# Performance work log

Hardware: AMD Instinct MI355X
Metric: run time of the kernel (lower is better)

Reference implementation:

```python
import jax, jax.numpy as jnp
import numpy as np
import math

NUM_HEADS = 8
RES_K = 9  # res_kernel_size


def setup_inputs() -> dict:
    key = jax.random.key(0)
    ks = jax.random.split(key, 6)
    N, C, h, w = 8, 256, 64, 64
    x = jax.random.normal(ks[0], (N, C, h, w), dtype=jnp.float32)
    w_qkv = jax.random.normal(ks[1], (3 * C, C), dtype=jnp.float32) * 0.02
    b_qkv = jax.random.normal(ks[2], (3 * C,), dtype=jnp.float32) * 0.02
    w_proj = jax.random.normal(ks[3], (C, C), dtype=jnp.float32) * 0.02
    b_proj = jax.random.normal(ks[4], (C,), dtype=jnp.float32) * 0.02
    w_dconv = jax.random.normal(ks[5], (NUM_HEADS, 1, RES_K, 1), dtype=jnp.float32) * 0.1
    return {"x": x, "w_qkv": w_qkv, "b_qkv": b_qkv,
            "w_proj": w_proj, "b_proj": b_proj, "w_dconv": w_dconv}


def _l2norm(t):
    # torch x / x.norm(dim=-1, keepdim=True): plain L2 norm, no eps
    return t / jnp.linalg.norm(t, axis=-1, keepdims=True)


def reference(x, w_qkv, b_qkv, w_proj, b_proj, w_dconv):
    N, C, h, w = x.shape
    H = NUM_HEADS
    D = C // H
    L = h * w
    xt = x.reshape(N, C, L).transpose(0, 2, 1)  # [N, L, C]
    qkv = xt @ w_qkv.T + b_qkv                   # [N, L, 3C]
    qkv = qkv.reshape(N, L, 3, H, D).transpose(2, 0, 3, 1, 4)  # [3, N, H, L, D]
    q, k, v = qkv[0], qkv[1], qkv[2]
    q = _l2norm(q)
    k = _l2norm(k)
    # depthwise conv over token dim: v as NCHW with C=H, H=L, W=D
    pad = RES_K // 2
    dconv_v = jax.lax.conv_general_dilated(
        v, w_dconv, window_strides=(1, 1), padding=[(pad, pad), (0, 0)],
        dimension_numbers=("NCHW", "OIHW", "NCHW"), feature_group_count=H)
    attn = jnp.einsum("nhld,nhle->nhde", k, v)   # [N, H, D, D]
    out = 0.5 * v + (1.0 / math.pi) * jnp.einsum("nhld,nhde->nhle", q, attn)
    out = _l2norm(out)
    out = out + dconv_v
    out = out.transpose(0, 2, 1, 3).reshape(N, L, C)  # [N, L, C]
    out = out @ w_proj.T + b_proj
    return out.transpose(0, 2, 1).reshape(N, C, h, w)
```

## Files before the change

### kernel.cpp

```cpp
#include <hip/hip_runtime.h>

#define NB 8
#define CC 256
#define HH 8
#define DD 32
#define LL 4096

typedef short v8s __attribute__((ext_vector_type(8)));
typedef float v4f __attribute__((ext_vector_type(4)));
typedef unsigned short v8u __attribute__((ext_vector_type(8)));
typedef unsigned short v4us __attribute__((ext_vector_type(4)));

__device__ __forceinline__ float4 ld4(const float* p) { return *(const float4*)p; }

__device__ __forceinline__ unsigned short f2bf(float f) {
    union { float f; unsigned int u; } v; v.f = f;
    unsigned int r = (v.u + 0x7FFFu + ((v.u >> 16) & 1u)) >> 16;
    return (unsigned short)r;
}
__device__ __forceinline__ float bf2f(unsigned short u) {
    union { unsigned int u; float f; } v; v.u = ((unsigned int)u) << 16;
    return v.f;
}

__device__ __forceinline__ void gl_lds16(const unsigned short* g, unsigned short* l) {
    __builtin_amdgcn_global_load_lds(
        (const __attribute__((address_space(1))) void*)g,
        (__attribute__((address_space(3))) void*)l, 16, 0, 0);
}

__global__ __launch_bounds__(256) void prep_w(
    const float* __restrict__ wq, const float* __restrict__ wp,
    unsigned short* __restrict__ dwq, unsigned short* __restrict__ dwp)
{
    int ti = blockIdx.x * 256 + threadIdx.x;
    if (ti < 24576) {
        int i = ti * 8;
        float4 f0 = ld4(wq + i), f1 = ld4(wq + i + 4);
        v8u o;
        o[0] = f2bf(f0.x); o[1] = f2bf(f0.y); o[2] = f2bf(f0.z); o[3] = f2bf(f0.w);
        o[4] = f2bf(f1.x); o[5] = f2bf(f1.y); o[6] = f2bf(f1.z); o[7] = f2bf(f1.w);
        *(v8u*)(dwq + i) = o;
    } else {
        int i = (ti - 24576) * 8;
        float4 f0 = ld4(wp + i), f1 = ld4(wp + i + 4);
        v8u o;
        o[0] = f2bf(f0.x); o[1] = f2bf(f0.y); o[2] = f2bf(f0.z); o[3] = f2bf(f0.w);
        o[4] = f2bf(f1.x); o[5] = f2bf(f1.y); o[6] = f2bf(f1.z); o[7] = f2bf(f1.w);
        *(v8u*)(dwp + i) = o;
    }
}

__global__ __launch_bounds__(256, 2) void gemm_qkv_mfma(
    const float* __restrict__ x, const unsigned short* __restrict__ wqb,
    const float* __restrict__ bqkv,
    unsigned short* __restrict__ q, unsigned short* __restrict__ k,
    unsigned short* __restrict__ v, float* __restrict__ attn)
{
    __shared__ __align__(16) unsigned short xsf[16384];
    __shared__ __align__(16) unsigned short wsb[16384];

    const int bid = blockIdx.x;
    const int l0 = (bid & 63) * 64;
    const int n  = bid >> 6;
    const int tid = threadIdx.x;
    const int lane = tid & 63, wave = tid >> 6;
    const int r = lane & 15, quad = lane >> 4;

    if (bid < 256) attn[bid * 256 + tid] = 0.f;

    {
        const int lx = tid & 63, cq = tid >> 6;
        const float* xcol = x + (size_t)n * CC * LL + l0 + lx;
        unsigned short* xrow = xsf + lx * 256;
#pragma unroll
        for (int i = 0; i < 8; ++i) {
            const float* src = xcol + (size_t)(cq * 8 + i) * 8 * LL;
            float f[8];
#pragma unroll
            for (int j = 0; j < 8; ++j) f[j] = src[(size_t)j * LL];
            v8u o;
#pragma unroll
            for (int j = 0; j < 8; ++j) o[j] = f2bf(f[j]);
            *(v8u*)(xrow + (cq * 8 + (i ^ (lx & 7))) * 8) = o;
        }
    }

    const int srow = wave * 8 + (lane >> 3);
    const int dchunk = (lane & 7) ^ (lane >> 3);
    unsigned short* wls = wsb + wave * 512 + lane * 8;
    const int jbase = wave * 64;

    for (int jt = 0; jt < 3; ++jt) {
        const int j0 = jt * 256;
        const unsigned short* wg = wqb + (size_t)(j0 + srow) * CC + dchunk * 8;

        v4f acc[4][4];
#pragma unroll
        for (int mi = 0; mi < 4; ++mi)
#pragma unroll
            for (int nj = 0; nj < 4; ++nj) acc[mi][nj] = (v4f)(0.f);

        for (int kt = 0; kt < 4; ++kt) {
            __syncthreads();
#pragma unroll
            for (int i = 0; i < 8; ++i)
                gl_lds16(wg + (size_t)i * 32 * CC + kt * 64, wls + i * 2048);
            __syncthreads();

#pragma unroll
            for (int kk = 0; kk < 2; ++kk) {
                const int cfrag = kk * 4 + quad;
                const int s = cfrag ^ (r & 7);
                v8s b[4];
#pragma unroll
                for (int nj = 0; nj < 4; ++nj)
                    b[nj] = *(const v8s*)(xsf + (nj * 16 + r) * 256 + kt * 64 + s * 8);
                v8s a[4];
#pragma unroll
                for (int mi = 0; mi < 4; ++mi)
                    a[mi] = *(const v8s*)(wsb + (jbase + mi * 16 + r) * 64 + s * 8);
#pragma unroll
                for (int mi = 0; mi < 4; ++mi)
#pragma unroll
                    for (int nj = 0; nj < 4; ++nj)
                        acc[mi][nj] = __builtin_amdgcn_mfma_f32_16x16x32_bf16(
                            a[mi], b[nj], acc[mi][nj], 0, 0, 0);
            }
        }

        unsigned short* basep = (jt == 0 ? q : (jt == 1 ? k : v));
        float bias[4][4];
#pragma unroll
        for (int mi = 0; mi < 4; ++mi)
            *(float4*)bias[mi] = *(const float4*)(bqkv + j0 + jbase + mi * 16 + quad * 4);

        unsigned short* dstp[4];
#pragma unroll
        for (int mi = 0; mi < 4; ++mi) {
            int hh = wave * 2 + (mi >> 1);
            int d0 = (mi & 1) * 16 + quad * 4;
            dstp[mi] = basep + (size_t)(n * HH + hh) * LL * DD + d0;
        }

        if (jt < 2) {
#pragma unroll
            for (int nj = 0; nj < 4; ++nj) {
                float t[4][4];
                float ss[2] = {0.f, 0.f};
#pragma unroll
                for (int mi = 0; mi < 4; ++mi)
#pragma unroll
                    for (int reg = 0; reg < 4; ++reg) {
                        float val = acc[mi][nj][reg] + bias[mi][reg];
                        t[mi][reg] = val;
                        ss[mi >> 1] += val * val;
                    }
#pragma unroll
                for (int g2 = 0; g2 < 2; ++g2) {
                    ss[g2] += __shfl_xor(ss[g2], 16);
                    ss[g2] += __shfl_xor(ss[g2], 32);
                    ss[g2] = rsqrtf(ss[g2]);
                }
                size_t l = (size_t)(l0 + nj * 16 + r);
#pragma unroll
                for (int mi = 0; mi < 4; ++mi) {
                    float rn = ss[mi >> 1];
                    v4us pk;
#pragma unroll
                    for (int reg = 0; reg < 4; ++reg) pk[reg] = f2bf(t[mi][reg] * rn);
                    *(v4us*)(dstp[mi] + l * DD) = pk;
                }
            }
        } else {
#pragma unroll
            for (int nj = 0; nj < 4; ++nj) {
                size_t l = (size_t)(l0 + nj * 16 + r);
#pragma unroll
                for (int mi = 0; mi < 4; ++mi) {
                    v4us pk;
#pragma unroll
                    for (int reg = 0; reg < 4; ++reg)
                        pk[reg] = f2bf(acc[mi][nj][reg] + bias[mi][reg]);
                    *(v4us*)(dstp[mi] + l * DD) = pk;
                }
            }
        }
    }
}

__global__ __launch_bounds__(256) void attn_k(
    const unsigned short* __restrict__ k, const unsigned short* __restrict__ v,
    float* __restrict__ attn)
{
    __shared__ float red[4][1024];
    const int nh = blockIdx.y;
    const int wv = threadIdx.x >> 6;
    const int lane = threadIdx.x & 63;
    const int eg = lane & 7;
    const int dg = lane >> 3;
    const int l0 = blockIdx.x * 512 + wv * 128;
    const unsigned short* kb = k + (size_t)nh * LL * DD;
    const unsigned short* vb = v + (size_t)nh * LL * DD;
    float acc[4][4] = {};
#pragma unroll 4
    for (int l = l0; l < l0 + 128; ++l) {
        v4us k4 = *(const v4us*)(kb + (size_t)l * DD + dg * 4);
        v4us v4 = *(const v4us*)(vb + (size_t)l * DD + eg * 4);
        float ka[4] = {bf2f(k4[0]), bf2f(k4[1]), bf2f(k4[2]), bf2f(k4[3])};
        float va[4] = {bf2f(v4[0]), bf2f(v4[1]), bf2f(v4[2]), bf2f(v4[3])};
#pragma unroll
        for (int dp = 0; dp < 4; ++dp)
#pragma unroll
            for (int ep = 0; ep < 4; ++ep)
                acc[dp][ep] += ka[dp] * va[ep];
    }
#pragma unroll
    for (int dp = 0; dp < 4; ++dp)
#pragma unroll
        for (int ep = 0; ep < 4; ++ep)
            red[wv][(dg * 4 + dp) * 32 + eg * 4 + ep] = acc[dp][ep];
    __syncthreads();
    float* ap = attn + (size_t)nh * 1024;
    for (int i = threadIdx.x; i < 1024; i += 256)
        atomicAdd(&ap[i], red[0][i] + red[1][i] + red[2][i] + red[3][i]);
}

#define PTOK 64
#define VTP 40
__global__ __launch_bounds__(256, 2) void midproj_k(
    const unsigned short* __restrict__ q, const unsigned short* __restrict__ v,
    const float* __restrict__ attn, const float* __restrict__ wd,
    const unsigned short* __restrict__ wpb, const float* __restrict__ bp,
    float* __restrict__ out)
{
    __shared__ __align__(16) unsigned short vt[8 * 72 * VTP];
    __shared__ __align__(16) unsigned short smid[4 * 64 * 64];

    const int n  = blockIdx.y;
    const int l0 = blockIdx.x * PTOK;
    const int tid = threadIdx.x;
    const int lane = tid & 63, wave = tid >> 6;
    const int r = lane & 15, quad = lane >> 4;

    const unsigned short* vbase = v + (size_t)(n * HH) * LL * DD;
#pragma unroll
    for (int it = 0; it < 9; ++it) {
        int task = it * 256 + tid;
        int seg = task & 3;
        int hr = task >> 2;
        int row = hr % 72;
        int h = hr / 72;
        int l = l0 - 4 + row;
        v8u val;
        if (l >= 0 && l < LL)
            val = *(const v8u*)(vbase + ((size_t)h * LL + l) * DD + seg * 8);
        else
            val = (v8u)(unsigned short)0;
        *(v8u*)(&vt[hr * VTP + seg * 8]) = val;
    }
    __syncthreads();

    const float inv_pi = 0.31830988618379067f;
#pragma unroll
    for (int hi = 0; hi < 2; ++hi) {
        const int h = wave * 2 + hi;
        const int nh = n * HH + h;
        const unsigned short* qb = q + (size_t)nh * LL * DD;
        const unsigned short* vth = vt + h * 72 * VTP;

        v8s bfrag[2];
#pragma unroll
        for (int et = 0; et < 2; ++et) {
            int e = et * 16 + r;
#pragma unroll
            for (int j = 0; j < 8; ++j)
                ((unsigned short*)&bfrag[et])[j] =
                    f2bf(attn[(size_t)nh * 1024 + (quad * 8 + j) * 32 + e]);
        }
        float wc[9];
#pragma unroll
        for (int r9 = 0; r9 < 9; ++r9) wc[r9] = wd[h * 9 + r9];

#pragma unroll
        for (int lt = 0; lt < 4; ++lt) {
            const int tb = lt * 16;
            v8s afrag = *(const v8s*)(qb + (size_t)(l0 + tb + r) * DD + quad * 8);
            v4f acc[2] = {(v4f)(0.f), (v4f)(0.f)};
#pragma unroll
            for (int et = 0; et < 2; ++et)
                acc[et] = __builtin_amdgcn_mfma_f32_16x16x32_bf16(
                    afrag, bfrag[et], acc[et], 0, 0, 0);

            float vcol[2][12];
#pragma unroll
            for (int et = 0; et < 2; ++et) {
                int e = et * 16 + r;
#pragma unroll
                for (int o = 0; o < 12; ++o)
                    vcol[et][o] = bf2f(vth[(tb + quad * 4 + o) * VTP + e]);
            }

            float t[2][4], ss[4];
#pragma unroll
            for (int reg = 0; reg < 4; ++reg) {
                t[0][reg] = 0.5f * vcol[0][4 + reg] + inv_pi * acc[0][reg];
                t[1][reg] = 0.5f * vcol[1][4 + reg] + inv_pi * acc[1][reg];
                ss[reg] = t[0][reg] * t[0][reg] + t[1][reg] * t[1][reg];
            }
#pragma unroll
            for (int m = 1; m < 16; m <<= 1)
#pragma unroll
                for (int reg = 0; reg < 4; ++reg)
                    ss[reg] += __shfl_xor(ss[reg], m);
#pragma unroll
            for (int reg = 0; reg < 4; ++reg) ss[reg] = rsqrtf(ss[reg]);

#pragma unroll
            for (int et = 0; et < 2; ++et) {
                int c = h * 32 + et * 16 + r;
                int chunk = c >> 6, c6 = c & 63;
                int goff = c6 & 7;
#pragma unroll
                for (int reg = 0; reg < 4; ++reg) {
                    float dv = 0.f;
#pragma unroll
                    for (int r9 = 0; r9 < 9; ++r9) dv += wc[r9] * vcol[et][reg + r9];
                    int l = tb + quad * 4 + reg;
                    int g = (c6 >> 3) ^ (l & 7);
                    smid[chunk * 4096 + l * 64 + g * 8 + goff] =
                        f2bf(t[et][reg] * ss[reg] + dv);
                }
            }
        }
    }
    __syncthreads();

    const int jbase = wave * 64;
    v4f acc[4][4];
#pragma unroll
    for (int mi = 0; mi < 4; ++mi)
#pragma unroll
        for (int nj = 0; nj < 4; ++nj) acc[mi][nj] = (v4f)(0.f);

#pragma unroll
    for (int kt = 0; kt < 4; ++kt) {
        v8s a[4][2], b[4][2];
#pragma unroll
        for (int kk = 0; kk < 2; ++kk) {
            const int cfrag = kk * 4 + quad;
#pragma unroll
            for (int mi = 0; mi < 4; ++mi) {
                int j = jbase + mi * 16 + r;
                a[mi][kk] = *(const v8s*)(wpb + (size_t)j * CC + kt * 64 + cfrag * 8);
            }
            const int s = cfrag ^ (r & 7);
#pragma unroll
            for (int nj = 0; nj < 4; ++nj) {
                int lloc = nj * 16 + r;
                b[nj][kk] = *(const v8s*)(smid + kt * 4096 + lloc * 64 + s * 8);
            }
        }
#pragma unroll
        for (int kk = 0; kk < 2; ++kk)
#pragma unroll
            for (int mi = 0; mi < 4; ++mi)
#pragma unroll
                for (int nj = 0; nj < 4; ++nj)
                    acc[mi][nj] = __builtin_amdgcn_mfma_f32_16x16x32_bf16(
                        a[mi][kk], b[nj][kk], acc[mi][nj], 0, 0, 0);
    }

#pragma unroll
    for (int mi = 0; mi < 4; ++mi)
#pragma unroll
        for (int reg = 0; reg < 4; ++reg) {
            int j = jbase + mi * 16 + quad * 4 + reg;
            float bias = bp[j];
#pragma unroll
            for (int nj = 0; nj < 4; ++nj) {
                int l = l0 + nj * 16 + r;
                out[((size_t)n * CC + j) * LL + l] = acc[mi][nj][reg] + bias;
            }
        }
}

extern "C" void kernel_launch(void* const* d_in, const int* in_sizes, int n_in,
                              void* d_out, int out_size, void* d_ws, size_t ws_size,
                              hipStream_t stream)
{
    const float* x     = (const float*)d_in[0];
    const float* wqkv  = (const float*)d_in[1];
    const float* bqkv  = (const float*)d_in[2];
    const float* wproj = (const float*)d_in[3];
    const float* bproj = (const float*)d_in[4];
    const float* wd    = (const float*)d_in[5];
    float* out = (float*)d_out;

    const size_t QKV = (size_t)NB * HH * LL * DD;
    unsigned short* q = (unsigned short*)d_ws;
    unsigned short* k = q + QKV;
    unsigned short* v = k + QKV;
    float* attn = (float*)(v + QKV);
    unsigned short* wqb = (unsigned short*)(attn + (size_t)NB * HH * DD * DD);
    unsigned short* wpb = wqb + 3 * CC * CC;

    prep_w<<<128, 256, 0, stream>>>(wqkv, wproj, wqb, wpb);
    gemm_qkv_mfma<<<512, 256, 0, stream>>>(x, wqb, bqkv, q, k, v, attn);
    attn_k<<<dim3(8, 64), 256, 0, stream>>>(k, v, attn);
    midproj_k<<<dim3(LL / PTOK, NB), 256, 0, stream>>>(q, v, attn, wd, wpb, bproj, out);
}
```

Baseline: 150.3 us.

## Double-buffer QKV weight tiles in LDS with prefetch of next K-slice

The QKV GEMM now streams weight tiles through two 8K-element LDS buffers in 32-wide K slices over 24 flattened steps. Each step issues the async global-to-LDS load for the next slice before computing the current one, so it needs one barrier per step instead of two. The first weight load is issued before the x-tile conversion so the two overlap. The cost is more barriers over a smaller K chunk per step and a fully unrolled 24-step loop, which grows code size. Correctness relies on a single barrier per step being enough for the async LDS writes to land before they are read.

```diff
diff --git a/kernel.cpp b/kernel.cpp
--- a/kernel.cpp
+++ b/kernel.cpp
@@ -51,6 +51,20 @@
     }
 }
 
+__device__ __forceinline__ void issue_w(
+    const unsigned short* __restrict__ wqb, unsigned short* wbuf_b,
+    int jt, int kt, int wave, int lane)
+{
+    const int wrow = lane >> 2;
+    const int wsc  = (lane & 3) ^ ((lane >> 3) & 3);
+    const unsigned short* wg = wqb + (size_t)(jt * 256 + wave * 64 + wrow) * CC
+                             + kt * 32 + wsc * 8;
+    unsigned short* wl = wbuf_b + wave * 2048 + lane * 8;
+#pragma unroll
+    for (int i = 0; i < 4; ++i)
+        gl_lds16(wg + (size_t)i * 16 * CC, wl + i * 512);
+}
+
 __global__ __launch_bounds__(256, 2) void gemm_qkv_mfma(
     const float* __restrict__ x, const unsigned short* __restrict__ wqb,
     const float* __restrict__ bqkv,
@@ -58,7 +72,7 @@
     unsigned short* __restrict__ v, float* __restrict__ attn)
 {
     __shared__ __align__(16) unsigned short xsf[16384];
-    __shared__ __align__(16) unsigned short wsb[16384];
+    __shared__ __align__(16) unsigned short wbuf[2][8192];
 
     const int bid = blockIdx.x;
     const int l0 = (bid & 63) * 64;
@@ -67,7 +81,7 @@
     const int lane = tid & 63, wave = tid >> 6;
     const int r = lane & 15, quad = lane >> 4;
 
-    if (bid < 256) attn[bid * 256 + tid] = 0.f;
+    issue_w(wqb, wbuf[0], 0, 0, wave, lane);
 
     {
         const int lx = tid & 63, cq = tid >> 6;
@@ -86,106 +100,106 @@
         }
     }
 
-    const int srow = wave * 8 + (lane >> 3);
-    const int dchunk = (lane & 7) ^ (lane >> 3);
-    unsigned short* wls = wsb + wave * 512 + lane * 8;
+    if (bid < 256) attn[bid * 256 + tid] = 0.f;
+
     const int jbase = wave * 64;
-
-    for (int jt = 0; jt < 3; ++jt) {
-        const int j0 = jt * 256;
-        const unsigned short* wg = wqb + (size_t)(j0 + srow) * CC + dchunk * 8;
-
-        v4f acc[4][4];
+    v4f acc[4][4];
+#pragma unroll
+    for (int mi = 0; mi < 4; ++mi)
+#pragma unroll
+        for (int nj = 0; nj < 4; ++nj) acc[mi][nj] = (v4f)(0.f);
+
+    int cur = 0;
+#pragma unroll
+    for (int t = 0; t < 24; ++t) {
+        __syncthreads();
+        if (t < 23)
+            issue_w(wqb, wbuf[cur ^ 1], (t + 1) >> 3, (t + 1) & 7, wave, lane);
+
+        const int kt = t & 7;
+        const int pos = (kt >> 1) * 8 + ((((kt & 1) << 2) + quad) ^ (r & 7));
+        v8s b[4];
+#pragma unroll
+        for (int nj = 0; nj < 4; ++nj)
+            b[nj] = *(const v8s*)(xsf + (nj * 16 + r) * 256 + pos * 8);
+        const int ws = (quad ^ ((r >> 1) & 3)) * 8;
+        v8s a[4];
 #pragma unroll
         for (int mi = 0; mi < 4; ++mi)
-#pragma unroll
-            for (int nj = 0; nj < 4; ++nj) acc[mi][nj] = (v4f)(0.f);
-
-        for (int kt = 0; kt < 4; ++kt) {
-            __syncthreads();
-#pragma unroll
-            for (int i = 0; i < 8; ++i)
-                gl_lds16(wg + (size_t)i * 32 * CC + kt * 64, wls + i * 2048);
-            __syncthreads();
-
-#pragma unroll
-            for (int kk = 0; kk < 2; ++kk) {
-                const int cfrag = kk * 4 + quad;
-                const int s = cfrag ^ (r & 7);
-                v8s b[4];
-#pragma unroll
-                for (int nj = 0; nj < 4; ++nj)
-                    b[nj] = *(const v8s*)(xsf + (nj * 16 + r) * 256 + kt * 64 + s * 8);
-                v8s a[4];
-#pragma unroll
-                for (int mi = 0; mi < 4; ++mi)
-                    a[mi] = *(const v8s*)(wsb + (jbase + mi * 16 + r) * 64 + s * 8);
-#pragma unroll
-                for (int mi = 0; mi < 4; ++mi)
-#pragma unroll
-                    for (int nj = 0; nj < 4; ++nj)
-                        acc[mi][nj] = __builtin_amdgcn_mfma_f32_16x16x32_bf16(
-                            a[mi], b[nj], acc[mi][nj], 0, 0, 0);
-            }
-        }
-
-        unsigned short* basep = (jt == 0 ? q : (jt == 1 ? k : v));
-        float bias[4][4];
+            a[mi] = *(const v8s*)(wbuf[cur] + (jbase + mi * 16 + r) * 32 + ws);
 #pragma unroll
         for (int mi = 0; mi < 4; ++mi)
-            *(float4*)bias[mi] = *(const float4*)(bqkv + j0 + jbase + mi * 16 + quad * 4);
-
-        unsigned short* dstp[4];
-#pragma unroll
-        for (int mi = 0; mi < 4; ++mi) {
-            int hh = wave * 2 + (mi >> 1);
-            int d0 = (mi & 1) * 16 + quad * 4;
-            dstp[mi] = basep + (size_t)(n * HH + hh) * LL * DD + d0;
-        }
-
-        if (jt < 2) {
-#pragma unroll
-            for (int nj = 0; nj < 4; ++nj) {
-                float t[4][4];
-                float ss[2] = {0.f, 0.f};
-#pragma unroll
-                for (int mi = 0; mi < 4; ++mi)
-#pragma unroll
-                    for (int reg = 0; reg < 4; ++reg) {
-                        float val = acc[mi][nj][reg] + bias[mi][reg];
-                        t[mi][reg] = val;
-                        ss[mi >> 1] += val * val;
+#pragma unroll
+            for (int nj = 0; nj < 4; ++nj)
+                acc[mi][nj] = __builtin_amdgcn_mfma_f32_16x16x32_bf16(
+                    a[mi], b[nj], acc[mi][nj], 0, 0, 0);
+
+        if ((t & 7) == 7) {
+            const int jt = t >> 3;
+            const int j0 = jt * 256;
+            unsigned short* basep = (jt == 0 ? q : (jt == 1 ? k : v));
+            float bias[4][4];
+#pragma unroll
+            for (int mi = 0; mi < 4; ++mi)
+                *(float4*)bias[mi] = *(const float4*)(bqkv + j0 + jbase + mi * 16 + quad * 4);
+
+            unsigned short* dstp[4];
+#pragma unroll
+            for (int mi = 0; mi < 4; ++mi) {
+                int hh = wave * 2 + (mi >> 1);
+                int d0 = (mi & 1) * 16 + quad * 4;
+                dstp[mi] = basep + (size_t)(n * HH + hh) * LL * DD + d0;
+            }
+
+            if (jt < 2) {
+#pragma unroll
+                for (int nj = 0; nj < 4; ++nj) {
+                    float t4[4][4];
+                    float ss[2] = {0.f, 0.f};
+#pragma unroll
+                    for (int mi = 0; mi < 4; ++mi)
+#pragma unroll
+                        for (int reg = 0; reg < 4; ++reg) {
+                            float val = acc[mi][nj][reg] + bias[mi][reg];
+                            t4[mi][reg] = val;
+                            ss[mi >> 1] += val * val;
+                        }
+#pragma unroll
+                    for (int g2 = 0; g2 < 2; ++g2) {
+                        ss[g2] += __shfl_xor(ss[g2], 16);
+                        ss[g2] += __shfl_xor(ss[g2], 32);
+                        ss[g2] = rsqrtf(ss[g2]);
                     }
-#pragma unroll
-                for (int g2 = 0; g2 < 2; ++g2) {
-                    ss[g2] += __shfl_xor(ss[g2], 16);
-                    ss[g2] += __shfl_xor(ss[g2], 32);
-                    ss[g2] = rsqrtf(ss[g2]);
+                    size_t l = (size_t)(l0 + nj * 16 + r);
+#pragma unroll
+                    for (int mi = 0; mi < 4; ++mi) {
+                        float rn = ss[mi >> 1];
+                        v4us pk;
+#pragma unroll
+                        for (int reg = 0; reg < 4; ++reg) pk[reg] = f2bf(t4[mi][reg] * rn);
+                        *(v4us*)(dstp[mi] + l * DD) = pk;
+                    }
                 }
-                size_t l = (size_t)(l0 + nj * 16 + r);
-#pragma unroll
-                for (int mi = 0; mi < 4; ++mi) {
-                    float rn = ss[mi >> 1];
-                    v4us pk;
-#pragma unroll
-                    for (int reg = 0; reg < 4; ++reg) pk[reg] = f2bf(t[mi][reg] * rn);
-                    *(v4us*)(dstp[mi] + l * DD) = pk;
+            } else {
+#pragma unroll
+                for (int nj = 0; nj < 4; ++nj) {
+                    size_t l = (size_t)(l0 + nj * 16 + r);
+#pragma unroll
+                    for (int mi = 0; mi < 4; ++mi) {
+                        v4us pk;
+#pragma unroll
+                        for (int reg = 0; reg < 4; ++reg)
+                            pk[reg] = f2bf(acc[mi][nj][reg] + bias[mi][reg]);
+                        *(v4us*)(dstp[mi] + l * DD) = pk;
+                    }
                 }
             }
-        } else {
-#pragma unroll
-            for (int nj = 0; nj < 4; ++nj) {
-                size_t l = (size_t)(l0 + nj * 16 + r);
-#pragma unroll
-                for (int mi = 0; mi < 4; ++mi) {
-                    v4us pk;
-#pragma unroll
-                    for (int reg = 0; reg < 4; ++reg)
-                        pk[reg] = f2bf(acc[mi][nj][reg] + bias[mi][reg]);
-                    *(v4us*)(dstp[mi] + l * DD) = pk;
-                }
-            }
-        }
+#pragma unroll
+            for (int mi = 0; mi < 4; ++mi)
+#pragma unroll
+                for (int nj = 0; nj < 4; ++nj) acc[mi][nj] = (v4f)(0.f);
+        }
+        cur ^= 1;
     }
 }
 
```

New measurement: 153.1 us. About the same (+1.9%).
